# Optimization experiments

Measured on AMD Instinct MI355X. Metric: run time of the kernel, lower is better.

Reference implementation:

```python
import jax, jax.numpy as jnp
import numpy as np

NUM_RELATIONS = 8
N_NODES = 50000
N_EDGES = 640000
D_IN = 128
D_HID = 128
N_CLASSES = 16


def rgcn_layer(x, edge_index, edge_type, edge_weight, W):
    # Faithful to ExtendedRGCNConv.forward: per-relation propagate with
    # message = (edge_weight * x_j) @ W[rel]  (== edge_weight * (x_j @ W[rel]))
    # aggregated by scatter-MEAN (PyG RGCNConv default aggr), summed over relations.
    # No root weight / bias (the override skips them).
    src, dst = edge_index[0], edge_index[1]
    num_nodes = x.shape[0]
    out = jnp.zeros((num_nodes, W.shape[2]), dtype=x.dtype)
    for r in range(W.shape[0]):
        sel = edge_type == r
        w = jnp.where(sel, edge_weight, jnp.zeros((), x.dtype))  # [E]
        h = x @ W[r]                                             # [N, out]
        msg = h[src] * w[:, None]                                # [E, out]
        s = jax.ops.segment_sum(msg, dst, num_segments=num_nodes)
        cnt = jax.ops.segment_sum(sel.astype(x.dtype), dst, num_segments=num_nodes)
        out = out + s / jnp.maximum(cnt, 1.0)[:, None]
    return out


def setup_inputs() -> dict:
    key = jax.random.key(0)
    k1, k2, k3, k4, k5, k6 = jax.random.split(key, 6)
    x = jax.random.normal(k1, (N_NODES, D_IN), dtype=jnp.float32)
    edge_index = jax.random.randint(k2, (2, N_EDGES), 0, N_NODES, dtype=jnp.int64)
    edge_type = jax.random.randint(k3, (N_EDGES,), 0, NUM_RELATIONS, dtype=jnp.int64)
    edge_attr = jax.random.uniform(k4, (N_EDGES,), dtype=jnp.float32)
    # Xavier-uniform-ish relation weight banks
    b1 = (6.0 / (D_IN + D_HID)) ** 0.5
    W1 = jax.random.uniform(k5, (NUM_RELATIONS, D_IN, D_HID), minval=-b1, maxval=b1, dtype=jnp.float32)
    b2 = (6.0 / (D_HID + N_CLASSES)) ** 0.5
    W2 = jax.random.uniform(k6, (NUM_RELATIONS, D_HID, N_CLASSES), minval=-b2, maxval=b2, dtype=jnp.float32)
    return {"x": x, "edge_index": edge_index, "edge_type": edge_type, "edge_attr": edge_attr, "W1": W1, "W2": W2}


def reference(x, edge_index, edge_type, edge_attr, W1, W2):
    h = rgcn_layer(x, edge_index, edge_type, edge_attr, W1)
    h = jax.nn.relu(h)
    h = rgcn_layer(h, edge_index, edge_type, edge_attr, W2)
    return jax.nn.log_softmax(h, axis=1)
```

## Files before the change

kernel.cpp:

```cpp
#include <hip/hip_runtime.h>
#include <hip/hip_bf16.h>
#include <math.h>

#define NN 50000
#define EE 640000
#define DD 128
#define NREL 8
#define NCLS 16
#define NBUCK (NREL * NN)
#define RECCAP 40
#define OSTR 12

typedef __attribute__((ext_vector_type(8))) short short8;
typedef __attribute__((ext_vector_type(4))) float f32x4;

__device__ __forceinline__ float bflo(unsigned u) { return __uint_as_float(u << 16); }
__device__ __forceinline__ float bfhi(unsigned u) { return __uint_as_float(u & 0xffff0000u); }
__device__ __forceinline__ float bf2f(ushort u) { return __uint_as_float(((unsigned)u) << 16); }
__device__ __forceinline__ ushort f2b(float f) {
  unsigned u = __float_as_uint(f);
  u += 0x7fff + ((u >> 16) & 1);
  return (ushort)(u >> 16);
}

#define XQ (NN * DD / 4)
#define PACKB ((XQ + DD * DD) / 256)
__global__ __launch_bounds__(256) void countpack_kernel(const int* __restrict__ ei,
                                                        const int* __restrict__ et,
                                                        const float* __restrict__ x,
                                                        const float* __restrict__ W1,
                                                        const float* __restrict__ W2,
                                                        int* __restrict__ cnt,
                                                        ushort* __restrict__ xb,
                                                        ushort* __restrict__ W1Tc,
                                                        ushort* __restrict__ W2T) {
  const int b = blockIdx.x;
  if (b < PACKB) {
    int t = b * 256 + threadIdx.x;
    if (t < EE) {
      int key = ei[EE + t] * NREL + et[t];
      atomicAdd(&cnt[key], 1);
    }
    if (t < XQ) {
      float4 v = *(const float4*)&x[(size_t)t * 4];
      *(ushort4*)&xb[(size_t)t * 4] = make_ushort4(f2b(v.x), f2b(v.y), f2b(v.z), f2b(v.w));
    } else {
      int t2 = t - XQ;
      int j = t2 >> 7, k = t2 & 127;
      W2T[t2] = f2b(W2[(j >> 4) * (DD * NCLS) + k * NCLS + (j & 15)]);
    }
  } else {
    __shared__ float lt[32][33];
    const int bb = b - PACKB;
    const int r = bb >> 4;
    const int tile = bb & 15;
    const int tk = (tile >> 2) * 32, tn = (tile & 3) * 32;
    const int lj = threadIdx.x & 31, li8 = threadIdx.x >> 5;
#pragma unroll
    for (int p = 0; p < 4; p++) {
      int i = p * 8 + li8;
      lt[i][lj] = W1[r * 16384 + (tk + i) * 128 + (tn + lj)];
    }
    __syncthreads();
#pragma unroll
    for (int p = 0; p < 4; p++) {
      int i = p * 8 + li8;
      W1Tc[(size_t)(tn + i) * 1024 + r * 128 + tk + lj] = f2b(lt[lj][i]);
    }
  }
}

__global__ __launch_bounds__(256) void base_kernel(int* __restrict__ cnt,
                                                   int* __restrict__ gcur,
                                                   int* __restrict__ offN) {
  const int v = blockIdx.x * 256 + threadIdx.x;
  const int lane = threadIdx.x & 63;
  int pre[9];
  pre[0] = 0;
  int deg = 0;
  if (v < NN) {
    int4 c0 = *(const int4*)&cnt[v * 8];
    int4 c1 = *(const int4*)&cnt[v * 8 + 4];
    pre[1] = pre[0] + c0.x;
    pre[2] = pre[1] + c0.y;
    pre[3] = pre[2] + c0.z;
    pre[4] = pre[3] + c0.w;
    pre[5] = pre[4] + c1.x;
    pre[6] = pre[5] + c1.y;
    pre[7] = pre[6] + c1.z;
    pre[8] = pre[7] + c1.w;
    deg = pre[8];
  } else {
#pragma unroll
    for (int i = 1; i < 9; i++) pre[i] = 0;
  }
  int incl = deg;
#pragma unroll
  for (int o = 1; o < 64; o <<= 1) {
    int t = __shfl_up(incl, o, 64);
    if (lane >= o) incl += t;
  }
  int wtotal = __shfl(incl, 63, 64);
  int wbase = 0;
  if (lane == 63) wbase = atomicAdd(gcur, wtotal);
  wbase = __shfl(wbase, 63, 64);
  if (v < NN) {
    int nbase = wbase + incl - deg;
#pragma unroll
    for (int i = 0; i < 9; i++) offN[v * OSTR + i] = nbase + pre[i];
#pragma unroll
    for (int r = 0; r < 8; r++) cnt[v * 8 + r] = nbase + pre[r + 1];
  }
}

__global__ __launch_bounds__(256) void bucket_kernel(const int* __restrict__ ei,
                                                     const int* __restrict__ et,
                                                     const float* __restrict__ ew,
                                                     int* __restrict__ cnt,
                                                     uint2* __restrict__ rec) {
  int e = blockIdx.x * 256 + threadIdx.x;
  if (e >= EE) return;
  int r = et[e];
  int key = ei[EE + e] * NREL + r;
  int pos = atomicSub(&cnt[key], 1) - 1;
  rec[pos] = make_uint2((unsigned)ei[e] | ((unsigned)r << 16), __float_as_uint(ew[e]));
}

__global__ __launch_bounds__(512) void fused1_kernel(const int* __restrict__ offN,
                                                     const uint2* __restrict__ rec,
                                                     const ushort* __restrict__ xb,
                                                     const ushort* __restrict__ W1Tc,
                                                     const ushort* __restrict__ W2T,
                                                     ushort* __restrict__ H2) {
  __shared__ ushort AsU[64 * 136];
  __shared__ uint2 recL[64 * RECCAP];
  const int tid = threadIdx.x;
  const int m0 = blockIdx.x * 64;
  const int wave = tid >> 6, lane = tid & 63;
  const int lm = lane & 15, lkb = (lane >> 4) * 8;
  const int gn = tid >> 3;
  const int gj = tid & 7;
  const int gc = gj * 16;
  const int v = m0 + gn;

  int offv[9];
  if (v < NN) {
    int4 o0 = *(const int4*)&offN[v * OSTR];
    int4 o1 = *(const int4*)&offN[v * OSTR + 4];
    offv[0] = o0.x; offv[1] = o0.y; offv[2] = o0.z; offv[3] = o0.w;
    offv[4] = o1.x; offv[5] = o1.y; offv[6] = o1.z; offv[7] = o1.w;
    offv[8] = offN[v * OSTR + 8];
  } else {
#pragma unroll
    for (int i = 0; i < 9; i++) offv[i] = 0;
  }
  const int b0 = offv[0];
  const int rbase = gn * RECCAP;
  {
    int dcap = min(offv[8] - b0, RECCAP);
    for (int i = gj; i < dcap; i += 8) recL[rbase + i] = rec[b0 + i];
  }

#define GETREC(qdst, ii)                                        \
  do {                                                          \
    int _ri = (ii) - b0;                                        \
    if (_ri < RECCAP) qdst = recL[rbase + _ri];                 \
    else qdst = rec[(ii)];                                      \
  } while (0)

  f32x4 acc[4];
#pragma unroll
  for (int m = 0; m < 4; m++) acc[m] = (f32x4){0.f, 0.f, 0.f, 0.f};

#pragma unroll
  for (int r = 0; r < NREL; r++) {
    __syncthreads();
    float g[16];
#pragma unroll
    for (int j = 0; j < 16; j++) g[j] = 0.f;
    const int s = offv[r], e = offv[r + 1];
    const float inv = 1.0f / fmaxf((float)(e - s), 1.0f);
    {
      int i = s;
      for (; i + 2 <= e; i += 2) {
        uint2 q0, q1;
        GETREC(q0, i);
        GETREC(q1, i + 1);
        float sc0 = __uint_as_float(q0.y), sc1 = __uint_as_float(q1.y);
        const ushort* xr0 = &xb[(size_t)(q0.x & 0xffff) * DD + gc];
        const ushort* xr1 = &xb[(size_t)(q1.x & 0xffff) * DD + gc];
        uint4 h0[2], h1[2];
#pragma unroll
        for (int jj = 0; jj < 2; jj++) h0[jj] = *(const uint4*)&xr0[jj * 8];
#pragma unroll
        for (int jj = 0; jj < 2; jj++) h1[jj] = *(const uint4*)&xr1[jj * 8];
#pragma unroll
        for (int jj = 0; jj < 2; jj++) {
          float* gg = &g[jj * 8];
          gg[0] = fmaf(sc0, bflo(h0[jj].x), gg[0]);
          gg[1] = fmaf(sc0, bfhi(h0[jj].x), gg[1]);
          gg[2] = fmaf(sc0, bflo(h0[jj].y), gg[2]);
          gg[3] = fmaf(sc0, bfhi(h0[jj].y), gg[3]);
          gg[4] = fmaf(sc0, bflo(h0[jj].z), gg[4]);
          gg[5] = fmaf(sc0, bfhi(h0[jj].z), gg[5]);
          gg[6] = fmaf(sc0, bflo(h0[jj].w), gg[6]);
          gg[7] = fmaf(sc0, bfhi(h0[jj].w), gg[7]);
          gg[0] = fmaf(sc1, bflo(h1[jj].x), gg[0]);
          gg[1] = fmaf(sc1, bfhi(h1[jj].x), gg[1]);
          gg[2] = fmaf(sc1, bflo(h1[jj].y), gg[2]);
          gg[3] = fmaf(sc1, bfhi(h1[jj].y), gg[3]);
          gg[4] = fmaf(sc1, bflo(h1[jj].z), gg[4]);
          gg[5] = fmaf(sc1, bfhi(h1[jj].z), gg[5]);
          gg[6] = fmaf(sc1, bflo(h1[jj].w), gg[6]);
          gg[7] = fmaf(sc1, bfhi(h1[jj].w), gg[7]);
        }
      }
      if (i < e) {
        uint2 q;
        GETREC(q, i);
        float sc = __uint_as_float(q.y);
        const ushort* xr = &xb[(size_t)(q.x & 0xffff) * DD + gc];
#pragma unroll
        for (int jj = 0; jj < 2; jj++) {
          uint4 h = *(const uint4*)&xr[jj * 8];
          float* gg = &g[jj * 8];
          gg[0] = fmaf(sc, bflo(h.x), gg[0]);
          gg[1] = fmaf(sc, bfhi(h.x), gg[1]);
          gg[2] = fmaf(sc, bflo(h.y), gg[2]);
          gg[3] = fmaf(sc, bfhi(h.y), gg[3]);
          gg[4] = fmaf(sc, bflo(h.z), gg[4]);
          gg[5] = fmaf(sc, bfhi(h.z), gg[5]);
          gg[6] = fmaf(sc, bflo(h.w), gg[6]);
          gg[7] = fmaf(sc, bfhi(h.w), gg[7]);
        }
      }
    }
#pragma unroll
    for (int jj = 0; jj < 2; jj++) {
      uint4 u;
      u.x = (unsigned)f2b(g[jj * 8 + 0] * inv) | ((unsigned)f2b(g[jj * 8 + 1] * inv) << 16);
      u.y = (unsigned)f2b(g[jj * 8 + 2] * inv) | ((unsigned)f2b(g[jj * 8 + 3] * inv) << 16);
      u.z = (unsigned)f2b(g[jj * 8 + 4] * inv) | ((unsigned)f2b(g[jj * 8 + 5] * inv) << 16);
      u.w = (unsigned)f2b(g[jj * 8 + 6] * inv) | ((unsigned)f2b(g[jj * 8 + 7] * inv) << 16);
      *(uint4*)&AsU[gn * 136 + gc + jj * 8] = u;
    }
    __syncthreads();
#pragma unroll
    for (int k0 = 0; k0 < 128; k0 += 32) {
      short8 b = *(const short8*)&W1Tc[(size_t)(wave * 16 + lm) * 1024 + r * 128 + k0 + lkb];
      short8 a[4];
#pragma unroll
      for (int m = 0; m < 4; m++)
        a[m] = *(const short8*)&AsU[(m * 16 + lm) * 136 + k0 + lkb];
#pragma unroll
      for (int m = 0; m < 4; m++)
        acc[m] = __builtin_amdgcn_mfma_f32_16x16x32_bf16(a[m], b, acc[m], 0, 0, 0);
    }
  }
#undef GETREC

  __syncthreads();
  const int rquad = (lane >> 4) * 4;
#pragma unroll
  for (int m = 0; m < 4; m++)
#pragma unroll
    for (int i = 0; i < 4; i++)
      AsU[(m * 16 + rquad + i) * 136 + wave * 16 + lm] = f2b(fmaxf(acc[m][i], 0.f));
  __syncthreads();

  f32x4 acc2[4];
#pragma unroll
  for (int m = 0; m < 4; m++) acc2[m] = (f32x4){0.f, 0.f, 0.f, 0.f};
#pragma unroll
  for (int k0 = 0; k0 < 128; k0 += 32) {
    short8 b = *(const short8*)&W2T[(size_t)(wave * 16 + lm) * DD + k0 + lkb];
    short8 a[4];
#pragma unroll
    for (int m = 0; m < 4; m++)
      a[m] = *(const short8*)&AsU[(m * 16 + lm) * 136 + k0 + lkb];
#pragma unroll
    for (int m = 0; m < 4; m++)
      acc2[m] = __builtin_amdgcn_mfma_f32_16x16x32_bf16(a[m], b, acc2[m], 0, 0, 0);
  }
  __syncthreads();
#pragma unroll
  for (int m = 0; m < 4; m++)
#pragma unroll
    for (int i = 0; i < 4; i++)
      AsU[(m * 16 + rquad + i) * 136 + wave * 16 + lm] = f2b(acc2[m][i]);
  __syncthreads();
#pragma unroll
  for (int i = 0; i < 2; i++) {
    int seg = tid + i * 512;
    int row = seg >> 4, c8 = (seg & 15) * 8;
    int gr = m0 + row;
    if (gr < NN) *(uint4*)&H2[(size_t)gr * DD + c8] = *(const uint4*)&AsU[row * 136 + c8];
  }
}

__global__ __launch_bounds__(256) void gather2_kernel(const int* __restrict__ offN,
                                                      const uint2* __restrict__ rec,
                                                      const ushort* __restrict__ H2,
                                                      float* __restrict__ out) {
  __shared__ uint2 recL[8 * RECCAP];
  __shared__ float invL[8][8];
  const int tid = threadIdx.x;
  const int g = tid >> 5;
  const int sub = tid & 31;
  const int j = sub >> 4;
  const int c = sub & 15;
  const int v = blockIdx.x * 8 + g;
  int s = 0, e = 0;
  if (v < NN) {
    s = offN[v * OSTR];
    e = offN[v * OSTR + 8];
  }
  if (sub < 8) {
    float cnt = 0.f;
    if (v < NN) cnt = (float)(offN[v * OSTR + sub + 1] - offN[v * OSTR + sub]);
    invL[g][sub] = 1.0f / fmaxf(cnt, 1.0f);
  }
  const int rbase = g * RECCAP;
  {
    int dcap = min(e - s, RECCAP);
    for (int i = sub; i < dcap; i += 32) recL[rbase + i] = rec[s + i];
  }
  __syncthreads();

#define GETREC2(qdst, ii)                                       \
  do {                                                          \
    int _ri = (ii) - s;                                         \
    if (_ri < RECCAP) qdst = recL[rbase + _ri];                 \
    else qdst = rec[(ii)];                                      \
  } while (0)

  float acc = 0.f;
  if (v < NN) {
    int i = s + j;
    for (; i + 2 < e; i += 4) {
      uint2 q0, q1;
      GETREC2(q0, i);
      GETREC2(q1, i + 2);
      ushort h0 = H2[(size_t)(q0.x & 0xffff) * DD + (q0.x >> 16) * NCLS + c];
      ushort h1 = H2[(size_t)(q1.x & 0xffff) * DD + (q1.x >> 16) * NCLS + c];
      acc = fmaf(__uint_as_float(q0.y) * invL[g][q0.x >> 16], bf2f(h0), acc);
      acc = fmaf(__uint_as_float(q1.y) * invL[g][q1.x >> 16], bf2f(h1), acc);
    }
    for (; i < e; i += 2) {
      uint2 q;
      GETREC2(q, i);
      acc = fmaf(__uint_as_float(q.y) * invL[g][q.x >> 16],
                 bf2f(H2[(size_t)(q.x & 0xffff) * DD + (q.x >> 16) * NCLS + c]), acc);
    }
  }
#undef GETREC2
  acc += __shfl_xor(acc, 16, 32);
  float m = acc;
#pragma unroll
  for (int mask = 8; mask >= 1; mask >>= 1) m = fmaxf(m, __shfl_xor(m, mask, 16));
  float ex = expf(acc - m);
#pragma unroll
  for (int mask = 8; mask >= 1; mask >>= 1) ex += __shfl_xor(ex, mask, 16);
  if (v < NN && j == 0) out[(size_t)v * NCLS + c] = acc - m - logf(ex);
}

extern "C" void kernel_launch(void* const* d_in, const int* in_sizes, int n_in,
                              void* d_out, int out_size, void* d_ws, size_t ws_size,
                              hipStream_t stream) {
  const float* x  = (const float*)d_in[0];
  const int*   ei = (const int*)d_in[1];
  const int*   et = (const int*)d_in[2];
  const float* ew = (const float*)d_in[3];
  const float* W1 = (const float*)d_in[4];
  const float* W2 = (const float*)d_in[5];
  float* out = (float*)d_out;
  float* ws = (float*)d_ws;

  int*    cnt  = (int*)ws;
  int*    gcur = (int*)(ws + 400000);
  int*    offN = (int*)(ws + 400004);
  uint2*  rec  = (uint2*)(ws + 1000004);
  ushort* xb   = (ushort*)(ws + 2280004);
  ushort* W1Tc = (ushort*)(ws + 5480004);
  ushort* W2T  = (ushort*)(ws + 5545540);
  ushort* H2   = (ushort*)(ws + 5553732);

  hipMemsetAsync(cnt, 0, (size_t)(NBUCK + 1) * sizeof(int), stream);

  countpack_kernel<<<PACKB + 128, 256, 0, stream>>>(ei, et, x, W1, W2, cnt, xb, W1Tc, W2T);
  base_kernel<<<(NN + 255) / 256, 256, 0, stream>>>(cnt, gcur, offN);
  bucket_kernel<<<(EE + 255) / 256, 256, 0, stream>>>(ei, et, ew, cnt, rec);

  fused1_kernel<<<(NN + 63) / 64, 512, 0, stream>>>(offN, rec, xb, W1Tc, W2T, H2);
  gather2_kernel<<<(NN + 7) / 8, 256, 0, stream>>>(offN, rec, H2, out);
}
```

Before: 250.7 us.

## Merge memset, count, scan and bucket into one cooperative kernel with grid syncs

Replaces the memset and three preprocessing kernels (count/pack, base scan, bucket fill) with a single cooperative kernel of 1024 blocks that uses grid-wide syncs between phases, removing launch gaps and the separate memset. The grid-stride loops and a fixed grid size change the work distribution, and grid.sync adds barrier cost. It also folds the mean normalization into each edge's weight scale instead of applying it after accumulation. The gcur counter is now zeroed inside the kernel along with cnt, and waves with zero total skip the atomic.

```diff
diff --git a/kernel.cpp b/kernel.cpp
--- a/kernel.cpp
+++ b/kernel.cpp
@@ -1,6 +1,9 @@
 #include <hip/hip_runtime.h>
 #include <hip/hip_bf16.h>
+#include <hip/hip_cooperative_groups.h>
 #include <math.h>
+
+namespace cg = cooperative_groups;
 
 #define NN 50000
 #define EE 640000
@@ -10,6 +13,8 @@
 #define NBUCK (NREL * NN)
 #define RECCAP 40
 #define OSTR 12
+#define CGRID 1024
+#define CNT (CGRID * 256)
 
 typedef __attribute__((ext_vector_type(8))) short short8;
 typedef __attribute__((ext_vector_type(4))) float f32x4;
@@ -24,19 +29,28 @@
 }
 
 #define XQ (NN * DD / 4)
-#define PACKB ((XQ + DD * DD) / 256)
-__global__ __launch_bounds__(256) void countpack_kernel(const int* __restrict__ ei,
-                                                        const int* __restrict__ et,
-                                                        const float* __restrict__ x,
-                                                        const float* __restrict__ W1,
-                                                        const float* __restrict__ W2,
-                                                        int* __restrict__ cnt,
-                                                        ushort* __restrict__ xb,
-                                                        ushort* __restrict__ W1Tc,
-                                                        ushort* __restrict__ W2T) {
-  const int b = blockIdx.x;
-  if (b < PACKB) {
-    int t = b * 256 + threadIdx.x;
+#define PACKN (XQ + DD * DD)
+__global__ __launch_bounds__(256, 4) void build_kernel(const int* __restrict__ ei,
+                                                       const int* __restrict__ et,
+                                                       const float* __restrict__ x,
+                                                       const float* __restrict__ W1,
+                                                       const float* __restrict__ W2,
+                                                       const float* __restrict__ ew,
+                                                       int* __restrict__ cnt,
+                                                       int* __restrict__ gcur,
+                                                       int* __restrict__ offN,
+                                                       uint2* __restrict__ rec,
+                                                       ushort* __restrict__ xb,
+                                                       ushort* __restrict__ W1Tc,
+                                                       ushort* __restrict__ W2T) {
+  cg::grid_group grid = cg::this_grid();
+  __shared__ float lt[32][33];
+  const int tid0 = blockIdx.x * 256 + threadIdx.x;
+
+  for (int i = tid0; i < NBUCK + 1; i += CNT) cnt[i] = 0;
+  grid.sync();
+
+  for (int t = tid0; t < PACKN; t += CNT) {
     if (t < EE) {
       int key = ei[EE + t] * NREL + et[t];
       atomicAdd(&cnt[key], 1);
@@ -49,9 +63,9 @@
       int j = t2 >> 7, k = t2 & 127;
       W2T[t2] = f2b(W2[(j >> 4) * (DD * NCLS) + k * NCLS + (j & 15)]);
     }
-  } else {
-    __shared__ float lt[32][33];
-    const int bb = b - PACKB;
+  }
+  if (blockIdx.x >= CGRID - 128) {
+    const int bb = blockIdx.x - (CGRID - 128);
     const int r = bb >> 4;
     const int tile = bb & 15;
     const int tk = (tile >> 2) * 32, tn = (tile & 3) * 32;
@@ -68,62 +82,58 @@
       W1Tc[(size_t)(tn + i) * 1024 + r * 128 + tk + lj] = f2b(lt[lj][i]);
     }
   }
-}
-
-__global__ __launch_bounds__(256) void base_kernel(int* __restrict__ cnt,
-                                                   int* __restrict__ gcur,
-                                                   int* __restrict__ offN) {
-  const int v = blockIdx.x * 256 + threadIdx.x;
-  const int lane = threadIdx.x & 63;
-  int pre[9];
-  pre[0] = 0;
-  int deg = 0;
-  if (v < NN) {
-    int4 c0 = *(const int4*)&cnt[v * 8];
-    int4 c1 = *(const int4*)&cnt[v * 8 + 4];
-    pre[1] = pre[0] + c0.x;
-    pre[2] = pre[1] + c0.y;
-    pre[3] = pre[2] + c0.z;
-    pre[4] = pre[3] + c0.w;
-    pre[5] = pre[4] + c1.x;
-    pre[6] = pre[5] + c1.y;
-    pre[7] = pre[6] + c1.z;
-    pre[8] = pre[7] + c1.w;
-    deg = pre[8];
-  } else {
-#pragma unroll
-    for (int i = 1; i < 9; i++) pre[i] = 0;
-  }
-  int incl = deg;
-#pragma unroll
-  for (int o = 1; o < 64; o <<= 1) {
-    int t = __shfl_up(incl, o, 64);
-    if (lane >= o) incl += t;
-  }
-  int wtotal = __shfl(incl, 63, 64);
-  int wbase = 0;
-  if (lane == 63) wbase = atomicAdd(gcur, wtotal);
-  wbase = __shfl(wbase, 63, 64);
-  if (v < NN) {
-    int nbase = wbase + incl - deg;
-#pragma unroll
-    for (int i = 0; i < 9; i++) offN[v * OSTR + i] = nbase + pre[i];
-#pragma unroll
-    for (int r = 0; r < 8; r++) cnt[v * 8 + r] = nbase + pre[r + 1];
-  }
-}
-
-__global__ __launch_bounds__(256) void bucket_kernel(const int* __restrict__ ei,
-                                                     const int* __restrict__ et,
-                                                     const float* __restrict__ ew,
-                                                     int* __restrict__ cnt,
-                                                     uint2* __restrict__ rec) {
-  int e = blockIdx.x * 256 + threadIdx.x;
-  if (e >= EE) return;
-  int r = et[e];
-  int key = ei[EE + e] * NREL + r;
-  int pos = atomicSub(&cnt[key], 1) - 1;
-  rec[pos] = make_uint2((unsigned)ei[e] | ((unsigned)r << 16), __float_as_uint(ew[e]));
+  grid.sync();
+
+  {
+    const int v = tid0;
+    const int lane = threadIdx.x & 63;
+    int pre[9];
+    pre[0] = 0;
+    int deg = 0;
+    if (v < NN) {
+      int4 c0 = *(const int4*)&cnt[v * 8];
+      int4 c1 = *(const int4*)&cnt[v * 8 + 4];
+      pre[1] = pre[0] + c0.x;
+      pre[2] = pre[1] + c0.y;
+      pre[3] = pre[2] + c0.z;
+      pre[4] = pre[3] + c0.w;
+      pre[5] = pre[4] + c1.x;
+      pre[6] = pre[5] + c1.y;
+      pre[7] = pre[6] + c1.z;
+      pre[8] = pre[7] + c1.w;
+      deg = pre[8];
+    } else {
+#pragma unroll
+      for (int i = 1; i < 9; i++) pre[i] = 0;
+    }
+    int incl = deg;
+#pragma unroll
+    for (int o = 1; o < 64; o <<= 1) {
+      int t = __shfl_up(incl, o, 64);
+      if (lane >= o) incl += t;
+    }
+    int wtotal = __shfl(incl, 63, 64);
+    int wbase = 0;
+    if (wtotal > 0) {
+      if (lane == 63) wbase = atomicAdd(gcur, wtotal);
+      wbase = __shfl(wbase, 63, 64);
+    }
+    if (v < NN) {
+      int nbase = wbase + incl - deg;
+#pragma unroll
+      for (int i = 0; i < 9; i++) offN[v * OSTR + i] = nbase + pre[i];
+#pragma unroll
+      for (int r = 0; r < 8; r++) cnt[v * 8 + r] = nbase + pre[r + 1];
+    }
+  }
+  grid.sync();
+
+  for (int e = tid0; e < EE; e += CNT) {
+    int r = et[e];
+    int key = ei[EE + e] * NREL + r;
+    int pos = atomicSub(&cnt[key], 1) - 1;
+    rec[pos] = make_uint2((unsigned)ei[e] | ((unsigned)r << 16), __float_as_uint(ew[e]));
+  }
 }
 
 __global__ __launch_bounds__(512) void fused1_kernel(const int* __restrict__ offN,
@@ -186,7 +196,7 @@
         uint2 q0, q1;
         GETREC(q0, i);
         GETREC(q1, i + 1);
-        float sc0 = __uint_as_float(q0.y), sc1 = __uint_as_float(q1.y);
+        float sc0 = __uint_as_float(q0.y) * inv, sc1 = __uint_as_float(q1.y) * inv;
         const ushort* xr0 = &xb[(size_t)(q0.x & 0xffff) * DD + gc];
         const ushort* xr1 = &xb[(size_t)(q1.x & 0xffff) * DD + gc];
         uint4 h0[2], h1[2];
@@ -218,7 +228,7 @@
       if (i < e) {
         uint2 q;
         GETREC(q, i);
-        float sc = __uint_as_float(q.y);
+        float sc = __uint_as_float(q.y) * inv;
         const ushort* xr = &xb[(size_t)(q.x & 0xffff) * DD + gc];
 #pragma unroll
         for (int jj = 0; jj < 2; jj++) {
@@ -238,10 +248,10 @@
 #pragma unroll
     for (int jj = 0; jj < 2; jj++) {
       uint4 u;
-      u.x = (unsigned)f2b(g[jj * 8 + 0] * inv) | ((unsigned)f2b(g[jj * 8 + 1] * inv) << 16);
-      u.y = (unsigned)f2b(g[jj * 8 + 2] * inv) | ((unsigned)f2b(g[jj * 8 + 3] * inv) << 16);
-      u.z = (unsigned)f2b(g[jj * 8 + 4] * inv) | ((unsigned)f2b(g[jj * 8 + 5] * inv) << 16);
-      u.w = (unsigned)f2b(g[jj * 8 + 6] * inv) | ((unsigned)f2b(g[jj * 8 + 7] * inv) << 16);
+      u.x = (unsigned)f2b(g[jj * 8 + 0]) | ((unsigned)f2b(g[jj * 8 + 1]) << 16);
+      u.y = (unsigned)f2b(g[jj * 8 + 2]) | ((unsigned)f2b(g[jj * 8 + 3]) << 16);
+      u.z = (unsigned)f2b(g[jj * 8 + 4]) | ((unsigned)f2b(g[jj * 8 + 5]) << 16);
+      u.w = (unsigned)f2b(g[jj * 8 + 6]) | ((unsigned)f2b(g[jj * 8 + 7]) << 16);
       *(uint4*)&AsU[gn * 136 + gc + jj * 8] = u;
     }
     __syncthreads();
@@ -367,9 +377,9 @@
 extern "C" void kernel_launch(void* const* d_in, const int* in_sizes, int n_in,
                               void* d_out, int out_size, void* d_ws, size_t ws_size,
                               hipStream_t stream) {
-  const float* x  = (const float*)d_in[0];
   const int*   ei = (const int*)d_in[1];
   const int*   et = (const int*)d_in[2];
+  const float* x  = (const float*)d_in[0];
   const float* ew = (const float*)d_in[3];
   const float* W1 = (const float*)d_in[4];
   const float* W2 = (const float*)d_in[5];
@@ -385,11 +395,11 @@
   ushort* W2T  = (ushort*)(ws + 5545540);
   ushort* H2   = (ushort*)(ws + 5553732);
 
-  hipMemsetAsync(cnt, 0, (size_t)(NBUCK + 1) * sizeof(int), stream);
-
-  countpack_kernel<<<PACKB + 128, 256, 0, stream>>>(ei, et, x, W1, W2, cnt, xb, W1Tc, W2T);
-  base_kernel<<<(NN + 255) / 256, 256, 0, stream>>>(cnt, gcur, offN);
-  bucket_kernel<<<(EE + 255) / 256, 256, 0, stream>>>(ei, et, ew, cnt, rec);
+  void* bargs[] = {(void*)&ei, (void*)&et, (void*)&x, (void*)&W1, (void*)&W2, (void*)&ew,
+                   (void*)&cnt, (void*)&gcur, (void*)&offN, (void*)&rec,
+                   (void*)&xb, (void*)&W1Tc, (void*)&W2T};
+  hipLaunchCooperativeKernel((const void*)build_kernel, dim3(CGRID), dim3(256),
+                             bargs, 0, stream);
 
   fused1_kernel<<<(NN + 63) / 64, 512, 0, stream>>>(offN, rec, xb, W1Tc, W2T, H2);
   gather2_kernel<<<(NN + 7) / 8, 256, 0, stream>>>(offN, rec, H2, out);
```

Measured after the change: 540.6 us. 2.16x slower.
